# Kernel tuning notes

Hardware: AMD Instinct MI355X
Metric: run time of the kernel (lower is better)

## Reference

```python
import jax, jax.numpy as jnp
import numpy as np

N, E, F_IN, F_HID, F_EMB, N_CLS = 50000, 800000, 100, 100, 64, 40


def setup_inputs() -> dict:
    key = jax.random.key(0)
    ks = jax.random.split(key, 8)
    x = jax.random.normal(ks[0], (N, F_IN), dtype=jnp.float32)
    edge_index = jax.random.randint(ks[1], (2, E), 0, N, dtype=jnp.int32)
    W1 = jax.random.normal(ks[2], (F_IN, F_HID), dtype=jnp.float32) / np.sqrt(F_IN)
    b1 = jnp.zeros((F_HID,), dtype=jnp.float32)
    W2 = jax.random.normal(ks[3], (F_HID, F_EMB), dtype=jnp.float32) / np.sqrt(F_HID)
    b2 = jnp.zeros((F_EMB,), dtype=jnp.float32)
    Wc = jax.random.normal(ks[4], (F_EMB, N_CLS), dtype=jnp.float32) / np.sqrt(F_EMB)
    bc = jnp.zeros((N_CLS,), dtype=jnp.float32)
    return {"x": x, "edge_index": edge_index, "W1": W1, "b1": b1,
            "W2": W2, "b2": b2, "Wc": Wc, "bc": bc}


def _gcn_conv(x, W, b, src, dst, dinv):
    # linear transform then symmetric-normalized neighbor aggregation
    h = x @ W                                   # [N, out]
    norm = dinv[src] * dinv[dst]                # [E+N]
    msg = h[src] * norm[:, None]                # gather + scale (edge-wise)
    out = jax.ops.segment_sum(msg, dst, num_segments=x.shape[0])
    return out + b


def reference(x, edge_index, W1, b1, W2, b2, Wc, bc):
    x = x.astype(jnp.float32)
    n = x.shape[0]
    loop = jnp.arange(n, dtype=edge_index.dtype)
    src = jnp.concatenate([edge_index[0], loop])  # add self-loops (PyG GCNConv)
    dst = jnp.concatenate([edge_index[1], loop])
    # degree (with self-loops) and D^-1/2, shared by both conv layers
    deg = jax.ops.segment_sum(jnp.ones_like(dst, dtype=x.dtype), dst, num_segments=n)
    dinv = jnp.where(deg > 0, jax.lax.rsqrt(jnp.maximum(deg, 1e-12)), 0.0)
    h = jax.nn.relu(_gcn_conv(x, W1, b1, src, dst, dinv))   # dropout off (eval)
    h = _gcn_conv(h, W2, b2, src, dst, dinv)
    h = jax.nn.relu(h)                                      # dropout off (eval)
    return h @ Wc + bc
```

## Files before the change

### kernel.cpp

```cpp
#include <hip/hip_runtime.h>

#define FIN 100
#define FHID 100
#define FEMB 64
#define NCLS 40

#define BSH 6
#define NSEG 8
#define SEGCAP 224
#define CSTR 16

typedef __attribute__((ext_vector_type(8))) short short8;
typedef __attribute__((ext_vector_type(4))) float f32x4;

__device__ inline unsigned short f2bf(float f) {
    unsigned u = __float_as_uint(f);
    u += 0x7FFFu + ((u >> 16) & 1u);
    return (unsigned short)(u >> 16);
}
__device__ inline float bf2f(unsigned short s) {
    return __uint_as_float((unsigned)s << 16);
}
__device__ inline float4 bf4(ushort4 u) {
    return make_float4(bf2f(u.x), bf2f(u.y), bf2f(u.z), bf2f(u.w));
}

__global__ __launch_bounds__(256) void k_bucket_sort(const int* __restrict__ arena,
                                                     const int* __restrict__ cur,
                                                     int* __restrict__ gcounter,
                                                     int* __restrict__ rowptr,
                                                     int* __restrict__ rowend,
                                                     float* __restrict__ dinv,
                                                     int* __restrict__ src_sorted, int n) {
    const int b = blockIdx.x;
    __shared__ int cnt[64], off[64];
    __shared__ int base_sh;
    if (threadIdx.x < 64) cnt[threadIdx.x] = 0;
    __syncthreads();
    for (int s = 0; s < NSEG; ++s) {
        int len = cur[(b * NSEG + s) * CSTR];
        if (len > SEGCAP) len = SEGCAP;
        const int* seg = arena + (size_t)(b * NSEG + s) * SEGCAP;
        for (int idx = threadIdx.x; idx < len; idx += 256)
            atomicAdd(&cnt[seg[idx] & 63], 1);
    }
    __syncthreads();
    if (threadIdx.x == 0) {
        int run = 0;
        for (int j = 0; j < 64; ++j) { off[j] = run; run += cnt[j]; }
        base_sh = atomicAdd(gcounter, run);
    }
    __syncthreads();
    const int base = base_sh;
    if (threadIdx.x < 64) {
        int node = (b << BSH) + threadIdx.x;
        if (node < n) {
            int r0 = base + off[threadIdx.x];
            rowptr[node] = r0;
            rowend[node] = r0 + cnt[threadIdx.x];
            dinv[node] = rsqrtf((float)cnt[threadIdx.x] + 1.0f);
        }
    }
    __syncthreads();
    for (int s = 0; s < NSEG; ++s) {
        int len = cur[(b * NSEG + s) * CSTR];
        if (len > SEGCAP) len = SEGCAP;
        const int* seg = arena + (size_t)(b * NSEG + s) * SEGCAP;
        for (int idx = threadIdx.x; idx < len; idx += 256) {
            int v = seg[idx];
            int lpos = atomicAdd(&off[v & 63], 1);
            src_sorted[base + lpos] = v >> BSH;
        }
    }
}

template <int KIN, int KOUT, bool A_BF16, bool BIAS, bool OUT_BF16, bool SCATTER>
__global__ __launch_bounds__(256) void k_gemm_mfma(const void* __restrict__ A,
                                                   const float* __restrict__ W,
                                                   const float* __restrict__ bias,
                                                   void* __restrict__ C, int n,
                                                   const int* __restrict__ src,
                                                   const int* __restrict__ dst,
                                                   int* __restrict__ cur,
                                                   int* __restrict__ arena, int E) {
    constexpr int KP   = ((KIN + 31) / 32) * 32;
    constexpr int NT   = (KOUT + 15) / 16;
    constexpr int NTC  = NT * 16;
    constexpr int APAD = KP + 8;
    constexpr int NKC  = KP / 32;
    constexpr int TQ   = (NT + 1) / 2;
    constexpr int KQ4  = KIN / 4;

    __shared__ unsigned short Abf[128 * APAD];
    __shared__ unsigned short Wt[NTC * APAD];

    const int row0 = blockIdx.x * 128;
    const int tid = threadIdx.x;

    if constexpr (SCATTER) {
        const int stride = gridDim.x * 256;
        for (int e = blockIdx.x * 256 + tid; e < E; e += stride) {
            int d = dst[e];
            int b = d >> BSH;
            int slot = b * NSEG + ((e >> 8) & (NSEG - 1));
            int p = atomicAdd(&cur[slot * CSTR], 1);
            if (p < SEGCAP) arena[slot * SEGCAP + p] = (src[e] << BSH) | (d & 63);
        }
    }

    if constexpr (A_BF16) {
        const ushort4* A4 = (const ushort4*)A;
        for (int idx = tid; idx < 128 * KQ4; idx += 256) {
            int r = idx / KQ4;
            int kq = idx - r * KQ4;
            ushort4 v = make_ushort4(0, 0, 0, 0);
            if (row0 + r < n) v = A4[(size_t)(row0 + r) * KQ4 + kq];
            *(ushort4*)&Abf[r * APAD + kq * 4] = v;
        }
    } else {
        const float* Af = (const float*)A;
        for (int idx = tid; idx < 128 * KQ4; idx += 256) {
            int r = idx / KQ4;
            int kq = idx - r * KQ4;
            float4 v = make_float4(0.f, 0.f, 0.f, 0.f);
            if (row0 + r < n) v = ((const float4*)(Af + (size_t)(row0 + r) * KIN))[kq];
            ushort4 o;
            o.x = f2bf(v.x); o.y = f2bf(v.y); o.z = f2bf(v.z); o.w = f2bf(v.w);
            *(ushort4*)&Abf[r * APAD + kq * 4] = o;
        }
    }
    if (KP > KIN) {
        constexpr int PADW = (KP > KIN) ? (KP - KIN) : 1;
        for (int idx = tid; idx < 128 * PADW; idx += 256) {
            int r = idx / PADW;
            Abf[r * APAD + KIN + (idx - r * PADW)] = 0;
        }
    }
    for (int idx = tid; idx < KIN * NTC; idx += 256) {
        int k = idx / NTC;
        int c = idx - k * NTC;
        float v = (c < KOUT) ? W[(size_t)k * KOUT + c] : 0.f;
        Wt[c * APAD + k] = f2bf(v);
    }
    if (KP > KIN) {
        constexpr int PADW = (KP > KIN) ? (KP - KIN) : 1;
        for (int idx = tid; idx < NTC * PADW; idx += 256) {
            int c = idx / PADW;
            Wt[c * APAD + KIN + (idx - c * PADW)] = 0;
        }
    }
    __syncthreads();

    const int lane = tid & 63;
    const int w    = tid >> 6;
    const int m0   = (w >> 1) * 64;
    const int t0   = (w & 1) * TQ;
    const int tcnt = (NT - t0 < TQ) ? (NT - t0) : TQ;
    const int lm   = lane & 15;
    const int quad = lane >> 4;

    f32x4 acc[4][TQ];
    #pragma unroll
    for (int i = 0; i < 4; ++i)
        #pragma unroll
        for (int t = 0; t < TQ; ++t)
            acc[i][t] = (f32x4)(0.f);

    for (int kt = 0; kt < NKC; ++kt) {
        short8 a[4], b[TQ];
        #pragma unroll
        for (int i = 0; i < 4; ++i)
            a[i] = *(const short8*)&Abf[(m0 + i * 16 + lm) * APAD + kt * 32 + quad * 8];
        #pragma unroll
        for (int t = 0; t < TQ; ++t)
            if (t < tcnt)
                b[t] = *(const short8*)&Wt[((t0 + t) * 16 + lm) * APAD + kt * 32 + quad * 8];
        #pragma unroll
        for (int i = 0; i < 4; ++i)
            #pragma unroll
            for (int t = 0; t < TQ; ++t)
                if (t < tcnt)
                    acc[i][t] = __builtin_amdgcn_mfma_f32_16x16x32_bf16(a[i], b[t], acc[i][t], 0, 0, 0);
    }

    #pragma unroll
    for (int t = 0; t < TQ; ++t) {
        if (t >= tcnt) continue;
        int col = (t0 + t) * 16 + lm;
        if (col >= KOUT) continue;
        float bv = BIAS ? bias[col] : 0.f;
        #pragma unroll
        for (int i = 0; i < 4; ++i) {
            #pragma unroll
            for (int rg = 0; rg < 4; ++rg) {
                int row = row0 + m0 + i * 16 + quad * 4 + rg;
                if (row < n) {
                    float v = acc[i][t][rg] + bv;
                    if (OUT_BF16)
                        ((unsigned short*)C)[(size_t)row * KOUT + col] = f2bf(v);
                    else
                        ((float*)C)[(size_t)row * KOUT + col] = v;
                }
            }
        }
    }
}

template <int F>
__global__ __launch_bounds__(256) void k_agg_bf(const unsigned short* __restrict__ h,
                                                const int* __restrict__ rowptr,
                                                const int* __restrict__ rowend,
                                                const int* __restrict__ src_sorted,
                                                const float* __restrict__ dinv,
                                                const float* __restrict__ bias,
                                                unsigned short* __restrict__ out, int n) {
    const int G = F / 4;
    int gid = blockIdx.x * blockDim.x + threadIdx.x;
    if (gid >= n * G) return;
    int i = gid / G;
    int cq = gid % G;
    const ushort4* h4 = (const ushort4*)h;

    float4 acc = make_float4(0.f, 0.f, 0.f, 0.f);
    int e = rowptr[i];
    const int end = rowend[i];
    for (; e + 3 < end; e += 4) {
        int s0 = src_sorted[e];
        int s1 = src_sorted[e + 1];
        int s2 = src_sorted[e + 2];
        int s3 = src_sorted[e + 3];
        ushort4 u0 = h4[(size_t)s0 * G + cq];
        ushort4 u1 = h4[(size_t)s1 * G + cq];
        ushort4 u2 = h4[(size_t)s2 * G + cq];
        ushort4 u3 = h4[(size_t)s3 * G + cq];
        float n0 = dinv[s0], n1 = dinv[s1], n2 = dinv[s2], n3 = dinv[s3];
        float4 v0 = bf4(u0), v1 = bf4(u1), v2 = bf4(u2), v3 = bf4(u3);
        acc.x = fmaf(v0.x, n0, acc.x); acc.y = fmaf(v0.y, n0, acc.y);
        acc.z = fmaf(v0.z, n0, acc.z); acc.w = fmaf(v0.w, n0, acc.w);
        acc.x = fmaf(v1.x, n1, acc.x); acc.y = fmaf(v1.y, n1, acc.y);
        acc.z = fmaf(v1.z, n1, acc.z); acc.w = fmaf(v1.w, n1, acc.w);
        acc.x = fmaf(v2.x, n2, acc.x); acc.y = fmaf(v2.y, n2, acc.y);
        acc.z = fmaf(v2.z, n2, acc.z); acc.w = fmaf(v2.w, n2, acc.w);
        acc.x = fmaf(v3.x, n3, acc.x); acc.y = fmaf(v3.y, n3, acc.y);
        acc.z = fmaf(v3.z, n3, acc.z); acc.w = fmaf(v3.w, n3, acc.w);
    }
    for (; e < end; ++e) {
        int s0 = src_sorted[e];
        float n0 = dinv[s0];
        float4 v0 = bf4(h4[(size_t)s0 * G + cq]);
        acc.x = fmaf(v0.x, n0, acc.x); acc.y = fmaf(v0.y, n0, acc.y);
        acc.z = fmaf(v0.z, n0, acc.z); acc.w = fmaf(v0.w, n0, acc.w);
    }

    float d = dinv[i];
    float4 hv = bf4(h4[(size_t)i * G + cq]);
    float4 bv = *(const float4*)&bias[cq * 4];
    ushort4 st;
    st.x = f2bf(fmaxf(fmaf(d, fmaf(d, hv.x, acc.x), bv.x), 0.f));
    st.y = f2bf(fmaxf(fmaf(d, fmaf(d, hv.y, acc.y), bv.y), 0.f));
    st.z = f2bf(fmaxf(fmaf(d, fmaf(d, hv.z, acc.z), bv.z), 0.f));
    st.w = f2bf(fmaxf(fmaf(d, fmaf(d, hv.w, acc.w), bv.w), 0.f));
    ((ushort4*)out)[(size_t)i * G + cq] = st;
}

extern "C" void kernel_launch(void* const* d_in, const int* in_sizes, int n_in,
                              void* d_out, int out_size, void* d_ws, size_t ws_size,
                              hipStream_t stream) {
    const float* x  = (const float*)d_in[0];
    const int*   ei = (const int*)d_in[1];
    const float* W1 = (const float*)d_in[2];
    const float* b1 = (const float*)d_in[3];
    const float* W2 = (const float*)d_in[4];
    const float* b2 = (const float*)d_in[5];
    const float* Wc = (const float*)d_in[6];
    const float* bc = (const float*)d_in[7];
    float* out = (float*)d_out;

    const int N = in_sizes[0] / FIN;
    const int E = in_sizes[1] / 2;
    const int* src = ei;
    const int* dst = ei + E;
    const int NBK = (N + 63) >> BSH;

    auto align = [](size_t v) { return (v + 255) & ~(size_t)255; };
    char* ws = (char*)d_ws;
    const size_t cur_bytes = align((size_t)NBK * NSEG * CSTR * 4 + 256);
    int*   cur        = (int*)ws;   ws += cur_bytes;
    int*   gcounter   = cur + (size_t)NBK * NSEG * CSTR;
    int*   arena      = (int*)ws;   ws += align((size_t)NBK * NSEG * SEGCAP * 4);
    int*   rowptr     = (int*)ws;   ws += align((size_t)N * 4);
    int*   rowend     = (int*)ws;   ws += align((size_t)N * 4);
    int*   src_sorted = (int*)ws;   ws += align((size_t)E * 4);
    float* dinv       = (float*)ws; ws += align((size_t)N * 4);
    unsigned short* h1  = (unsigned short*)ws; ws += align((size_t)N * FHID * 2);
    unsigned short* a1r = (unsigned short*)ws; ws += align((size_t)N * FHID * 2);
    unsigned short* h2  = (unsigned short*)ws; ws += align((size_t)N * FEMB * 2);
    unsigned short* a2r = (unsigned short*)ws; ws += align((size_t)N * FEMB * 2);

    const int B = 256;
    const int nmb = (N + 127) / 128;

    hipMemsetAsync(cur, 0, cur_bytes, stream);

    k_gemm_mfma<FIN, FHID, false, false, true, true><<<nmb, B, 0, stream>>>(
        x, W1, nullptr, h1, N, src, dst, cur, arena, E);

    k_bucket_sort<<<NBK, B, 0, stream>>>(arena, cur, gcounter, rowptr, rowend, dinv, src_sorted, N);

    k_agg_bf<FHID><<<((size_t)N * (FHID / 4) + B - 1) / B, B, 0, stream>>>(
        h1, rowptr, rowend, src_sorted, dinv, b1, a1r, N);

    k_gemm_mfma<FHID, FEMB, true, false, true, false><<<nmb, B, 0, stream>>>(
        a1r, W2, nullptr, h2, N, nullptr, nullptr, nullptr, nullptr, 0);

    k_agg_bf<FEMB><<<((size_t)N * (FEMB / 4) + B - 1) / B, B, 0, stream>>>(
        h2, rowptr, rowend, src_sorted, dinv, b2, a2r, N);

    k_gemm_mfma<FEMB, NCLS, true, true, false, false><<<nmb, B, 0, stream>>>(
        a2r, Wc, bc, out, N, nullptr, nullptr, nullptr, nullptr, 0);
}
```

Baseline: 226.0 us.

## Fuse second aggregation with classifier GEMM and split first GEMM over columns

Adds a k_agg_gemm kernel that performs the layer-2 neighbor aggregation straight into shared memory and then runs the classifier MFMA GEMM. This removes the a2r intermediate round trip through global memory and one kernel launch. The first GEMM also gains a column-tile template parameter and now launches on a 2D grid with two column halves, so it runs twice as many blocks and each block keeps fewer accumulators. The trade-offs are that the aggregation in the fused kernel has per-block load imbalance and each block redundantly converts Wc, and the column split makes every block reload and reconvert the same A tile.

```diff
diff --git a/kernel.cpp b/kernel.cpp
--- a/kernel.cpp
+++ b/kernel.cpp
@@ -74,7 +74,7 @@
     }
 }
 
-template <int KIN, int KOUT, bool A_BF16, bool BIAS, bool OUT_BF16, bool SCATTER>
+template <int KIN, int KOUT, int NTY, bool A_BF16, bool BIAS, bool OUT_BF16, bool SCATTER>
 __global__ __launch_bounds__(256) void k_gemm_mfma(const void* __restrict__ A,
                                                    const float* __restrict__ W,
                                                    const float* __restrict__ bias,
@@ -83,23 +83,25 @@
                                                    const int* __restrict__ dst,
                                                    int* __restrict__ cur,
                                                    int* __restrict__ arena, int E) {
-    constexpr int KP   = ((KIN + 31) / 32) * 32;
-    constexpr int NT   = (KOUT + 15) / 16;
-    constexpr int NTC  = NT * 16;
-    constexpr int APAD = KP + 8;
-    constexpr int NKC  = KP / 32;
-    constexpr int TQ   = (NT + 1) / 2;
-    constexpr int KQ4  = KIN / 4;
+    constexpr int KP    = ((KIN + 31) / 32) * 32;
+    constexpr int NTALL = (KOUT + 15) / 16;
+    constexpr int NTC   = NTY * 16;
+    constexpr int APAD  = KP + 8;
+    constexpr int NKC   = KP / 32;
+    constexpr int TQ    = (NTY + 1) / 2;
+    constexpr int KQ4   = KIN / 4;
 
     __shared__ unsigned short Abf[128 * APAD];
     __shared__ unsigned short Wt[NTC * APAD];
 
-    const int row0 = blockIdx.x * 128;
+    const int row0  = blockIdx.x * 128;
+    const int tbase = blockIdx.y * NTY;
+    const int ntloc = (NTALL - tbase < NTY) ? (NTALL - tbase) : NTY;
     const int tid = threadIdx.x;
 
     if constexpr (SCATTER) {
-        const int stride = gridDim.x * 256;
-        for (int e = blockIdx.x * 256 + tid; e < E; e += stride) {
+        const int stride = gridDim.x * gridDim.y * 256;
+        for (int e = (blockIdx.y * gridDim.x + blockIdx.x) * 256 + tid; e < E; e += stride) {
             int d = dst[e];
             int b = d >> BSH;
             int slot = b * NSEG + ((e >> 8) & (NSEG - 1));
@@ -139,7 +141,8 @@
     for (int idx = tid; idx < KIN * NTC; idx += 256) {
         int k = idx / NTC;
         int c = idx - k * NTC;
-        float v = (c < KOUT) ? W[(size_t)k * KOUT + c] : 0.f;
+        int gc = tbase * 16 + c;
+        float v = (gc < KOUT) ? W[(size_t)k * KOUT + gc] : 0.f;
         Wt[c * APAD + k] = f2bf(v);
     }
     if (KP > KIN) {
@@ -155,7 +158,7 @@
     const int w    = tid >> 6;
     const int m0   = (w >> 1) * 64;
     const int t0   = (w & 1) * TQ;
-    const int tcnt = (NT - t0 < TQ) ? (NT - t0) : TQ;
+    const int tcnt = (ntloc - t0 < TQ) ? (ntloc - t0) : TQ;
     const int lm   = lane & 15;
     const int quad = lane >> 4;
 
@@ -186,7 +189,7 @@
     #pragma unroll
     for (int t = 0; t < TQ; ++t) {
         if (t >= tcnt) continue;
-        int col = (t0 + t) * 16 + lm;
+        int col = (tbase + t0 + t) * 16 + lm;
         if (col >= KOUT) continue;
         float bv = BIAS ? bias[col] : 0.f;
         #pragma unroll
@@ -263,6 +266,137 @@
     ((ushort4*)out)[(size_t)i * G + cq] = st;
 }
 
+template <int KIN, int KOUT>
+__global__ __launch_bounds__(256) void k_agg_gemm(const unsigned short* __restrict__ h,
+                                                  const int* __restrict__ rowptr,
+                                                  const int* __restrict__ rowend,
+                                                  const int* __restrict__ src_sorted,
+                                                  const float* __restrict__ dinv,
+                                                  const float* __restrict__ bias_agg,
+                                                  const float* __restrict__ W,
+                                                  const float* __restrict__ bias_out,
+                                                  float* __restrict__ C, int n) {
+    static_assert(KIN % 32 == 0, "KIN must be mult of 32 (no K-pad path here)");
+    constexpr int KP   = KIN;
+    constexpr int NT   = (KOUT + 15) / 16;
+    constexpr int NTC  = NT * 16;
+    constexpr int APAD = KP + 8;
+    constexpr int NKC  = KP / 32;
+    constexpr int TQ   = (NT + 1) / 2;
+    constexpr int G    = KIN / 4;
+
+    __shared__ unsigned short Abf[128 * APAD];
+    __shared__ unsigned short Wt[NTC * APAD];
+
+    const int row0 = blockIdx.x * 128;
+    const int tid = threadIdx.x;
+
+    for (int idx = tid; idx < KIN * NTC; idx += 256) {
+        int k = idx / NTC;
+        int c = idx - k * NTC;
+        float v = (c < KOUT) ? W[(size_t)k * KOUT + c] : 0.f;
+        Wt[c * APAD + k] = f2bf(v);
+    }
+
+    const ushort4* h4 = (const ushort4*)h;
+    for (int task = tid; task < 128 * G; task += 256) {
+        int r = task / G;
+        int cq = task - r * G;
+        int i = row0 + r;
+        ushort4 st = make_ushort4(0, 0, 0, 0);
+        if (i < n) {
+            float4 acc = make_float4(0.f, 0.f, 0.f, 0.f);
+            int e = rowptr[i];
+            const int end = rowend[i];
+            for (; e + 3 < end; e += 4) {
+                int s0 = src_sorted[e];
+                int s1 = src_sorted[e + 1];
+                int s2 = src_sorted[e + 2];
+                int s3 = src_sorted[e + 3];
+                ushort4 u0 = h4[(size_t)s0 * G + cq];
+                ushort4 u1 = h4[(size_t)s1 * G + cq];
+                ushort4 u2 = h4[(size_t)s2 * G + cq];
+                ushort4 u3 = h4[(size_t)s3 * G + cq];
+                float n0 = dinv[s0], n1 = dinv[s1], n2 = dinv[s2], n3 = dinv[s3];
+                float4 v0 = bf4(u0), v1 = bf4(u1), v2 = bf4(u2), v3 = bf4(u3);
+                acc.x = fmaf(v0.x, n0, acc.x); acc.y = fmaf(v0.y, n0, acc.y);
+                acc.z = fmaf(v0.z, n0, acc.z); acc.w = fmaf(v0.w, n0, acc.w);
+                acc.x = fmaf(v1.x, n1, acc.x); acc.y = fmaf(v1.y, n1, acc.y);
+                acc.z = fmaf(v1.z, n1, acc.z); acc.w = fmaf(v1.w, n1, acc.w);
+                acc.x = fmaf(v2.x, n2, acc.x); acc.y = fmaf(v2.y, n2, acc.y);
+                acc.z = fmaf(v2.z, n2, acc.z); acc.w = fmaf(v2.w, n2, acc.w);
+                acc.x = fmaf(v3.x, n3, acc.x); acc.y = fmaf(v3.y, n3, acc.y);
+                acc.z = fmaf(v3.z, n3, acc.z); acc.w = fmaf(v3.w, n3, acc.w);
+            }
+            for (; e < end; ++e) {
+                int s0 = src_sorted[e];
+                float n0 = dinv[s0];
+                float4 v0 = bf4(h4[(size_t)s0 * G + cq]);
+                acc.x = fmaf(v0.x, n0, acc.x); acc.y = fmaf(v0.y, n0, acc.y);
+                acc.z = fmaf(v0.z, n0, acc.z); acc.w = fmaf(v0.w, n0, acc.w);
+            }
+            float d = dinv[i];
+            float4 hv = bf4(h4[(size_t)i * G + cq]);
+            float4 bv = ((const float4*)bias_agg)[cq];
+            st.x = f2bf(fmaxf(fmaf(d, fmaf(d, hv.x, acc.x), bv.x), 0.f));
+            st.y = f2bf(fmaxf(fmaf(d, fmaf(d, hv.y, acc.y), bv.y), 0.f));
+            st.z = f2bf(fmaxf(fmaf(d, fmaf(d, hv.z, acc.z), bv.z), 0.f));
+            st.w = f2bf(fmaxf(fmaf(d, fmaf(d, hv.w, acc.w), bv.w), 0.f));
+        }
+        *(ushort4*)&Abf[r * APAD + cq * 4] = st;
+    }
+    __syncthreads();
+
+    const int lane = tid & 63;
+    const int w    = tid >> 6;
+    const int m0   = (w >> 1) * 64;
+    const int t0   = (w & 1) * TQ;
+    const int tcnt = (NT - t0 < TQ) ? (NT - t0) : TQ;
+    const int lm   = lane & 15;
+    const int quad = lane >> 4;
+
+    f32x4 acc[4][TQ];
+    #pragma unroll
+    for (int i = 0; i < 4; ++i)
+        #pragma unroll
+        for (int t = 0; t < TQ; ++t)
+            acc[i][t] = (f32x4)(0.f);
+
+    for (int kt = 0; kt < NKC; ++kt) {
+        short8 a[4], b[TQ];
+        #pragma unroll
+        for (int i = 0; i < 4; ++i)
+            a[i] = *(const short8*)&Abf[(m0 + i * 16 + lm) * APAD + kt * 32 + quad * 8];
+        #pragma unroll
+        for (int t = 0; t < TQ; ++t)
+            if (t < tcnt)
+                b[t] = *(const short8*)&Wt[((t0 + t) * 16 + lm) * APAD + kt * 32 + quad * 8];
+        #pragma unroll
+        for (int i = 0; i < 4; ++i)
+            #pragma unroll
+            for (int t = 0; t < TQ; ++t)
+                if (t < tcnt)
+                    acc[i][t] = __builtin_amdgcn_mfma_f32_16x16x32_bf16(a[i], b[t], acc[i][t], 0, 0, 0);
+    }
+
+    #pragma unroll
+    for (int t = 0; t < TQ; ++t) {
+        if (t >= tcnt) continue;
+        int col = (t0 + t) * 16 + lm;
+        if (col >= KOUT) continue;
+        float bv = bias_out[col];
+        #pragma unroll
+        for (int i = 0; i < 4; ++i) {
+            #pragma unroll
+            for (int rg = 0; rg < 4; ++rg) {
+                int row = row0 + m0 + i * 16 + quad * 4 + rg;
+                if (row < n)
+                    C[(size_t)row * KOUT + col] = acc[i][t][rg] + bv;
+            }
+        }
+    }
+}
+
 extern "C" void kernel_launch(void* const* d_in, const int* in_sizes, int n_in,
                               void* d_out, int out_size, void* d_ws, size_t ws_size,
                               hipStream_t stream) {
@@ -295,14 +429,13 @@
     unsigned short* h1  = (unsigned short*)ws; ws += align((size_t)N * FHID * 2);
     unsigned short* a1r = (unsigned short*)ws; ws += align((size_t)N * FHID * 2);
     unsigned short* h2  = (unsigned short*)ws; ws += align((size_t)N * FEMB * 2);
-    unsigned short* a2r = (unsigned short*)ws; ws += align((size_t)N * FEMB * 2);
 
     const int B = 256;
     const int nmb = (N + 127) / 128;
 
     hipMemsetAsync(cur, 0, cur_bytes, stream);
 
-    k_gemm_mfma<FIN, FHID, false, false, true, true><<<nmb, B, 0, stream>>>(
+    k_gemm_mfma<FIN, FHID, 4, false, false, true, true><<<dim3(nmb, 2), B, 0, stream>>>(
         x, W1, nullptr, h1, N, src, dst, cur, arena, E);
 
     k_bucket_sort<<<NBK, B, 0, stream>>>(arena, cur, gcounter, rowptr, rowend, dinv, src_sorted, N);
@@ -310,12 +443,9 @@
     k_agg_bf<FHID><<<((size_t)N * (FHID / 4) + B - 1) / B, B, 0, stream>>>(
         h1, rowptr, rowend, src_sorted, dinv, b1, a1r, N);
 
-    k_gemm_mfma<FHID, FEMB, true, false, true, false><<<nmb, B, 0, stream>>>(
+    k_gemm_mfma<FHID, FEMB, 4, true, false, true, false><<<dim3(nmb, 1), B, 0, stream>>>(
         a1r, W2, nullptr, h2, N, nullptr, nullptr, nullptr, nullptr, 0);
 
-    k_agg_bf<FEMB><<<((size_t)N * (FEMB / 4) + B - 1) / B, B, 0, stream>>>(
-        h2, rowptr, rowend, src_sorted, dinv, b2, a2r, N);
-
-    k_gemm_mfma<FEMB, NCLS, true, true, false, false><<<nmb, B, 0, stream>>>(
-        a2r, Wc, bc, out, N, nullptr, nullptr, nullptr, nullptr, 0);
-}
+    k_agg_gemm<FEMB, NCLS><<<nmb, B, 0, stream>>>(
+        h2, rowptr, rowend, src_sorted, dinv, b2, Wc, bc, out, N);
+}
```

New measurement: 269.1 us. 1.19x slower.
